# Optimization experiments

Hardware: AMD Instinct MI355X
Metric: run time of the kernel (lower is better)

The kernel has to match this reference:

```python
import jax, jax.numpy as jnp
import numpy as np

EPS = 1e-12
B, CNT = 4096, 2048

def setup_inputs() -> dict:
    key = jax.random.key(0)
    k1, k2, k3 = jax.random.split(key, 3)
    timestampns_set = jax.random.uniform(k1, (B, CNT), dtype=jnp.float32)
    gyro_set = jax.random.normal(k2, (B, CNT, 3), dtype=jnp.float32)
    start_quat = jax.random.normal(k3, (B, 4), dtype=jnp.float32)
    # conv1/conv2 reduce to 3x3 linear maps on the xyz axis; initialized to identity, bias 0
    W1 = jnp.eye(3, dtype=jnp.float32)
    b1 = jnp.zeros((3,), dtype=jnp.float32)
    a1 = jnp.float32(0.25)  # PReLU default, single shared parameter
    W2 = jnp.eye(3, dtype=jnp.float32)
    b2 = jnp.zeros((3,), dtype=jnp.float32)
    a2 = jnp.float32(0.25)
    return {"timestampns_set": timestampns_set, "gyro_set": gyro_set,
            "start_quat": start_quat, "W1": W1, "b1": b1, "a1": a1,
            "W2": W2, "b2": b2, "a2": a2}

def _prelu(x, a):
    return jnp.where(x >= 0, x, a * x)

def _qmul(a, b):
    aw, ax, ay, az = a[:, 0], a[:, 1], a[:, 2], a[:, 3]
    bw, bx, by, bz = b[:, 0], b[:, 1], b[:, 2], b[:, 3]
    ow = aw * bw - ax * bx - ay * by - az * bz
    ox = aw * bx + ax * bw + ay * bz - az * by
    oy = aw * by - ax * bz + ay * bw + az * bx
    oz = aw * bz + ax * by - ay * bx + az * bw
    return jnp.stack((ow, ox, oy, oz), axis=-1)

def reference(timestampns_set, gyro_set, start_quat, W1, b1, a1, W2, b2, a2):
    # calibrate_gyro: two identity-init 3x3 'convs' + PReLU, residual add
    h = _prelu(jnp.einsum('btc,oc->bto', gyro_set, W1) + b1, a1)
    g = _prelu(jnp.einsum('btc,oc->bto', h, W2) + b2, a2) + gyro_set  # [B,CNT,3]
    dt = timestampns_set[:, 1:] - timestampns_set[:, :-1]             # [B,CNT-1]
    gm = 0.5 * (g[:, :-1, :] + g[:, 1:, :])                            # midpoint gyro
    dtheta_half = gm * dt[:, :, None] * 0.5                           # [B,CNT-1,3]

    def step(q, d):
        dq = jnp.concatenate([jnp.ones((d.shape[0], 1), d.dtype), d], axis=1)
        q = _qmul(q, dq)
        n = jnp.sqrt(jnp.sum(q * q, axis=1, keepdims=True))
        q = q / jnp.maximum(n, EPS)  # F.normalize semantics
        return q, None

    q, _ = jax.lax.scan(step, start_quat, jnp.swapaxes(dtheta_half, 0, 1))
    return q
```

## Files before the change

kernel.cpp:

```cpp
#include <hip/hip_runtime.h>

#define CNT   2048
#define NSTEP 2047
#define TPB   256
#define CHUNK 8

struct Q { float w, x, y, z; };

__device__ inline Q qmul(const Q a, const Q b) {
    Q o;
    o.w = a.w*b.w - a.x*b.x - a.y*b.y - a.z*b.z;
    o.x = a.w*b.x + a.x*b.w + a.y*b.z - a.z*b.y;
    o.y = a.w*b.y - a.x*b.z + a.y*b.w + a.z*b.x;
    o.z = a.w*b.z + a.x*b.y - a.y*b.x + a.z*b.w;
    return o;
}

__global__ __launch_bounds__(TPB) void quat_scan_kernel(
    const float* __restrict__ ts,
    const float* __restrict__ gyro,
    const float* __restrict__ sq,
    const float* __restrict__ W1, const float* __restrict__ b1, const float* __restrict__ a1p,
    const float* __restrict__ W2, const float* __restrict__ b2, const float* __restrict__ a2p,
    float* __restrict__ out)
{
    __shared__ float s_g[CNT * 3];
    __shared__ float s_t[CNT];
    __shared__ Q     s_q[TPB];

    const int b   = blockIdx.x;
    const int tid = threadIdx.x;

    const float4* g4  = (const float4*)(gyro + (size_t)b * (CNT * 3));
    float4*       sg4 = (float4*)s_g;
    #pragma unroll
    for (int k = 0; k < 6; ++k) sg4[tid + k * TPB] = g4[tid + k * TPB];

    const float4* t4  = (const float4*)(ts + (size_t)b * CNT);
    float4*       st4 = (float4*)s_t;
    #pragma unroll
    for (int k = 0; k < 2; ++k) st4[tid + k * TPB] = t4[tid + k * TPB];

    float w1[9], w2[9], bb1[3], bb2[3];
    #pragma unroll
    for (int i = 0; i < 9; ++i) { w1[i] = W1[i]; w2[i] = W2[i]; }
    #pragma unroll
    for (int i = 0; i < 3; ++i) { bb1[i] = b1[i]; bb2[i] = b2[i]; }
    const float a1 = a1p[0], a2 = a2p[0];

    __syncthreads();

    auto gf = [&](int t, float& gx, float& gy, float& gz) {
        const float vx = s_g[3*t + 0], vy = s_g[3*t + 1], vz = s_g[3*t + 2];
        float h0 = w1[0]*vx + w1[1]*vy + w1[2]*vz + bb1[0];
        float h1 = w1[3]*vx + w1[4]*vy + w1[5]*vz + bb1[1];
        float h2 = w1[6]*vx + w1[7]*vy + w1[8]*vz + bb1[2];
        h0 = h0 >= 0.0f ? h0 : a1 * h0;
        h1 = h1 >= 0.0f ? h1 : a1 * h1;
        h2 = h2 >= 0.0f ? h2 : a1 * h2;
        float u0 = w2[0]*h0 + w2[1]*h1 + w2[2]*h2 + bb2[0];
        float u1 = w2[3]*h0 + w2[4]*h1 + w2[5]*h2 + bb2[1];
        float u2 = w2[6]*h0 + w2[7]*h1 + w2[8]*h2 + bb2[2];
        u0 = u0 >= 0.0f ? u0 : a2 * u0;
        u1 = u1 >= 0.0f ? u1 : a2 * u1;
        u2 = u2 >= 0.0f ? u2 : a2 * u2;
        gx = u0 + vx; gy = u1 + vy; gz = u2 + vz;
    };

    const int t0   = tid * CHUNK;
    int       tend = t0 + CHUNK;
    if (tend > NSTEP) tend = NSTEP;

    Q q = {1.0f, 0.0f, 0.0f, 0.0f};
    float g0x, g0y, g0z;
    gf(t0, g0x, g0y, g0z);
    for (int t = t0; t < tend; ++t) {
        float g1x, g1y, g1z;
        gf(t + 1, g1x, g1y, g1z);
        const float dt = s_t[t + 1] - s_t[t];
        const float s  = 0.25f * dt;
        const Q dq = {1.0f, (g0x + g1x) * s, (g0y + g1y) * s, (g0z + g1z) * s};
        q = qmul(q, dq);
        g0x = g1x; g0y = g1y; g0z = g1z;
    }

    {
        const float n2  = q.w*q.w + q.x*q.x + q.y*q.y + q.z*q.z;
        const float inv = 1.0f / sqrtf(n2);
        q.w *= inv; q.x *= inv; q.y *= inv; q.z *= inv;
    }

    s_q[tid] = q;
    __syncthreads();

    #pragma unroll
    for (int stride = 1; stride < TPB; stride <<= 1) {
        if ((tid & (2 * stride - 1)) == 0) {
            s_q[tid] = qmul(s_q[tid], s_q[tid + stride]);
        }
        __syncthreads();
    }

    if (tid == 0) {
        const float4 s0 = ((const float4*)(sq + (size_t)b * 4))[0];
        const Q q0 = {s0.x, s0.y, s0.z, s0.w};
        Q qf = qmul(q0, s_q[0]);
        const float n  = sqrtf(qf.w*qf.w + qf.x*qf.x + qf.y*qf.y + qf.z*qf.z);
        const float dn = fmaxf(n, 1e-12f);
        const float inv = 1.0f / dn;
        float4 o;
        o.x = qf.w * inv; o.y = qf.x * inv; o.z = qf.y * inv; o.w = qf.z * inv;
        ((float4*)(out + (size_t)b * 4))[0] = o;
    }
}

extern "C" void kernel_launch(void* const* d_in, const int* in_sizes, int n_in,
                              void* d_out, int out_size, void* d_ws, size_t ws_size,
                              hipStream_t stream) {
    const float* ts   = (const float*)d_in[0];
    const float* gyro = (const float*)d_in[1];
    const float* sq   = (const float*)d_in[2];
    const float* W1   = (const float*)d_in[3];
    const float* b1   = (const float*)d_in[4];
    const float* a1   = (const float*)d_in[5];
    const float* W2   = (const float*)d_in[6];
    const float* b2   = (const float*)d_in[7];
    const float* a2   = (const float*)d_in[8];
    float* out = (float*)d_out;

    const int B = in_sizes[0] / CNT;

    quat_scan_kernel<<<B, TPB, 0, stream>>>(ts, gyro, sq, W1, b1, a1, W2, b2, a2, out);
}
```

Baseline: 186.9 us.

## Load gyro chunks directly to registers and reduce quaternions with wave shuffles

Each thread now loads its own 8-step gyro and timestamp chunk, plus one halo sample, straight from global memory into registers. This replaces staging the whole row in shared memory, which drops 32KB of LDS per block and the first barrier, so more blocks can stay resident. The shared-memory tree reduction is replaced by a wave-level shuffle reduction followed by a short serial combine across the four waves. The per-step quaternion multiply is specialised for a unit real part, and the last thread pads its missing halo with zeros and a repeated timestamp. The per-thread global loads are strided, which may coalesce less well than the old row-wide loads.

```diff
diff --git a/kernel.cpp b/kernel.cpp
--- a/kernel.cpp
+++ b/kernel.cpp
@@ -4,6 +4,7 @@
 #define NSTEP 2047
 #define TPB   256
 #define CHUNK 8
+#define NWAVE (TPB / 64)
 
 struct Q { float w, x, y, z; };
 
@@ -16,6 +17,15 @@
     return o;
 }
 
+__device__ inline Q qmul1(const Q a, const float bx, const float by, const float bz) {
+    Q o;
+    o.w = a.w - (a.x*bx + a.y*by + a.z*bz);
+    o.x = a.x + (a.w*bx + a.y*bz - a.z*by);
+    o.y = a.y + (a.w*by - a.x*bz + a.z*bx);
+    o.z = a.z + (a.w*bz + a.x*by - a.y*bx);
+    return o;
+}
+
 __global__ __launch_bounds__(TPB) void quat_scan_kernel(
     const float* __restrict__ ts,
     const float* __restrict__ gyro,
@@ -24,22 +34,31 @@
     const float* __restrict__ W2, const float* __restrict__ b2, const float* __restrict__ a2p,
     float* __restrict__ out)
 {
-    __shared__ float s_g[CNT * 3];
-    __shared__ float s_t[CNT];
-    __shared__ Q     s_q[TPB];
+    __shared__ Q s_q[NWAVE];
 
-    const int b   = blockIdx.x;
-    const int tid = threadIdx.x;
+    const int b    = blockIdx.x;
+    const int tid  = threadIdx.x;
+    const int t0   = tid * CHUNK;
+    const bool last = (tid == TPB - 1);
 
-    const float4* g4  = (const float4*)(gyro + (size_t)b * (CNT * 3));
-    float4*       sg4 = (float4*)s_g;
-    #pragma unroll
-    for (int k = 0; k < 6; ++k) sg4[tid + k * TPB] = g4[tid + k * TPB];
-
-    const float4* t4  = (const float4*)(ts + (size_t)b * CNT);
-    float4*       st4 = (float4*)s_t;
-    #pragma unroll
-    for (int k = 0; k < 2; ++k) st4[tid + k * TPB] = t4[tid + k * TPB];
+    float rg[28];
+    {
+        const float4* gp = (const float4*)(gyro + (size_t)b * (CNT * 3) + (size_t)t0 * 3);
+        #pragma unroll
+        for (int k = 0; k < 6; ++k) ((float4*)rg)[k] = gp[k];
+        if (!last) {
+            ((float4*)rg)[6] = gp[6];
+        } else {
+            ((float4*)rg)[6] = make_float4(0.f, 0.f, 0.f, 0.f);
+        }
+    }
+    float rt[9];
+    {
+        const float4* tp = (const float4*)(ts + (size_t)b * CNT + t0);
+        #pragma unroll
+        for (int k = 0; k < 2; ++k) ((float4*)&rt[0])[k] = tp[k];
+        rt[8] = last ? rt[7] : ts[(size_t)b * CNT + t0 + 8];
+    }
 
     float w1[9], w2[9], bb1[3], bb2[3];
     #pragma unroll
@@ -48,10 +67,8 @@
     for (int i = 0; i < 3; ++i) { bb1[i] = b1[i]; bb2[i] = b2[i]; }
     const float a1 = a1p[0], a2 = a2p[0];
 
-    __syncthreads();
-
-    auto gf = [&](int t, float& gx, float& gy, float& gz) {
-        const float vx = s_g[3*t + 0], vy = s_g[3*t + 1], vz = s_g[3*t + 2];
+    auto gf = [&](int j, float& gx, float& gy, float& gz) {
+        const float vx = rg[3*j + 0], vy = rg[3*j + 1], vz = rg[3*j + 2];
         float h0 = w1[0]*vx + w1[1]*vy + w1[2]*vz + bb1[0];
         float h1 = w1[3]*vx + w1[4]*vy + w1[5]*vz + bb1[1];
         float h2 = w1[6]*vx + w1[7]*vy + w1[8]*vz + bb1[2];
@@ -67,20 +84,15 @@
         gx = u0 + vx; gy = u1 + vy; gz = u2 + vz;
     };
 
-    const int t0   = tid * CHUNK;
-    int       tend = t0 + CHUNK;
-    if (tend > NSTEP) tend = NSTEP;
-
     Q q = {1.0f, 0.0f, 0.0f, 0.0f};
     float g0x, g0y, g0z;
-    gf(t0, g0x, g0y, g0z);
-    for (int t = t0; t < tend; ++t) {
+    gf(0, g0x, g0y, g0z);
+    #pragma unroll
+    for (int j = 0; j < CHUNK; ++j) {
         float g1x, g1y, g1z;
-        gf(t + 1, g1x, g1y, g1z);
-        const float dt = s_t[t + 1] - s_t[t];
-        const float s  = 0.25f * dt;
-        const Q dq = {1.0f, (g0x + g1x) * s, (g0y + g1y) * s, (g0z + g1z) * s};
-        q = qmul(q, dq);
+        gf(j + 1, g1x, g1y, g1z);
+        const float s = 0.25f * (rt[j + 1] - rt[j]);
+        q = qmul1(q, (g0x + g1x) * s, (g0y + g1y) * s, (g0z + g1z) * s);
         g0x = g1x; g0y = g1y; g0z = g1z;
     }
 
@@ -90,24 +102,31 @@
         q.w *= inv; q.x *= inv; q.y *= inv; q.z *= inv;
     }
 
-    s_q[tid] = q;
+    #pragma unroll
+    for (int sft = 1; sft < 64; sft <<= 1) {
+        Q o;
+        o.w = __shfl_down(q.w, sft);
+        o.x = __shfl_down(q.x, sft);
+        o.y = __shfl_down(q.y, sft);
+        o.z = __shfl_down(q.z, sft);
+        q = qmul(q, o);
+    }
+
+    const int lane = tid & 63;
+    const int wid  = tid >> 6;
+    if (lane == 0) s_q[wid] = q;
     __syncthreads();
 
-    #pragma unroll
-    for (int stride = 1; stride < TPB; stride <<= 1) {
-        if ((tid & (2 * stride - 1)) == 0) {
-            s_q[tid] = qmul(s_q[tid], s_q[tid + stride]);
-        }
-        __syncthreads();
-    }
+    if (tid == 0) {
+        Q acc = s_q[0];
+        #pragma unroll
+        for (int w = 1; w < NWAVE; ++w) acc = qmul(acc, s_q[w]);
 
-    if (tid == 0) {
         const float4 s0 = ((const float4*)(sq + (size_t)b * 4))[0];
         const Q q0 = {s0.x, s0.y, s0.z, s0.w};
-        Q qf = qmul(q0, s_q[0]);
-        const float n  = sqrtf(qf.w*qf.w + qf.x*qf.x + qf.y*qf.y + qf.z*qf.z);
-        const float dn = fmaxf(n, 1e-12f);
-        const float inv = 1.0f / dn;
+        Q qf = qmul(q0, acc);
+        const float n   = sqrtf(qf.w*qf.w + qf.x*qf.x + qf.y*qf.y + qf.z*qf.z);
+        const float inv = 1.0f / fmaxf(n, 1e-12f);
         float4 o;
         o.x = qf.w * inv; o.y = qf.x * inv; o.z = qf.y * inv; o.w = qf.z * inv;
         ((float4*)(out + (size_t)b * 4))[0] = o;
```

After: 185.9 us. Within noise of the previous version (-0.6%).
